# Kernel tuning notes

Hardware: AMD Instinct MI355X
Metric: run time of the kernel (lower is better)

## Reference

```python
import jax, jax.numpy as jnp
import numpy as np

BATCH, N, DIM_IN, DIM_K, DIM_V, NH = 2, 4096, 256, 256, 256, 8

def setup_inputs() -> dict:
    key = jax.random.key(0)
    k1, k2, k3, k4 = jax.random.split(key, 4)
    s = 1.0 / np.sqrt(DIM_IN)
    return {
        "x": jax.random.normal(k1, (BATCH, N, DIM_IN), dtype=jnp.float32),
        "Wq": jax.random.normal(k2, (DIM_IN, DIM_K), dtype=jnp.float32) * s,
        "Wk": jax.random.normal(k3, (DIM_IN, DIM_K), dtype=jnp.float32) * s,
        "Wv": jax.random.normal(k4, (DIM_IN, DIM_V), dtype=jnp.float32) * s,
    }

def reference(x, Wq, Wk, Wv):
    b, n, _ = x.shape
    nh = NH
    dk = DIM_K // nh
    dv = DIM_V // nh
    # project and split heads: [b, nh, n, dk]
    q = jnp.einsum('bni,ik->bnk', x, Wq).reshape(b, n, nh, dk).transpose(0, 2, 1, 3)
    k = jnp.einsum('bni,ik->bnk', x, Wk).reshape(b, n, nh, dk).transpose(0, 2, 1, 3)
    v = jnp.einsum('bni,iv->bnv', x, Wv).reshape(b, n, nh, dv).transpose(0, 2, 1, 3)
    scale = 1.0 / np.sqrt(dk)
    dist = jnp.einsum('bhqd,bhkd->bhqk', q, k) * scale  # [b, nh, n, n]
    dist = jax.nn.softmax(dist, axis=-1)
    # dropout is identity in eval mode
    att = jnp.einsum('bhqk,bhkv->bhqv', dist, v)  # [b, nh, n, dv]
    return att.transpose(0, 2, 1, 3).reshape(b, n, DIM_V)
```

## Files before the change

kernel.cpp:

```cpp
#include <hip/hip_runtime.h>
#include <math.h>

#define BATCH 2
#define SEQ   4096
#define DIN   256
#define NH    8
#define DH    32
#define BH    (BATCH*NH)
#define NSPLIT 4
#define KRANGE (SEQ/NSPLIT)
#define TILES  (KRANGE/64)

typedef short bf16x8 __attribute__((ext_vector_type(8)));
typedef float f32x4  __attribute__((ext_vector_type(4)));

#if defined(__has_builtin)
#if __has_builtin(__builtin_amdgcn_exp2f)
#define EXP2(x) __builtin_amdgcn_exp2f(x)
#else
#define EXP2_ASM 1
#endif
#else
#define EXP2_ASM 1
#endif
#ifdef EXP2_ASM
__device__ __forceinline__ float exp2_raw(float x) {
    float r;
    asm("v_exp_f32 %0, %1\n\ts_nop 1" : "=v"(r) : "v"(x));
    return r;
}
#define EXP2(x) exp2_raw(x)
#endif

#define SC2 0.25508218f

__device__ __forceinline__ unsigned short f2bf(float f) {
    unsigned int u = __builtin_bit_cast(unsigned int, f);
    u += 0x7fffu + ((u >> 16) & 1u);
    return (unsigned short)(u >> 16);
}

__device__ __forceinline__ unsigned int pack_bf2(float f0, float f1) {
    unsigned int u0 = __builtin_bit_cast(unsigned int, f0) + 0x8000u;
    unsigned int u1 = __builtin_bit_cast(unsigned int, f1) + 0x8000u;
    return __builtin_amdgcn_perm(u1, u0, 0x07060302u);
}

__device__ __forceinline__ unsigned int pack_bf2_t(float f0, float f1) {
    return __builtin_amdgcn_perm(__builtin_bit_cast(unsigned int, f1),
                                 __builtin_bit_cast(unsigned int, f0),
                                 0x07060302u);
}

#if defined(__has_builtin)
#if __has_builtin(__builtin_amdgcn_global_load_lds)
#define HAS_ASYNC_LDS 1
#endif
#endif

__device__ __forceinline__ void stage16(const unsigned short* g,
                                        unsigned short* lds_base, int lane) {
#ifdef HAS_ASYNC_LDS
    __builtin_amdgcn_global_load_lds(
        (const __attribute__((address_space(1))) unsigned int*)g,
        (__attribute__((address_space(3))) unsigned int*)lds_base, 16, 0, 0);
#else
    *(bf16x8*)(lds_base + (size_t)lane * 8) = *(const bf16x8*)g;
#endif
}

__global__ __launch_bounds__(256) void prep_kernel(
    const float* __restrict__ x,
    const float* __restrict__ Wq, const float* __restrict__ Wk, const float* __restrict__ Wv,
    unsigned short* __restrict__ xb, unsigned short* __restrict__ Wt)
{
    const int t = threadIdx.x;
    if (blockIdx.x < 2048) {
        int i4 = blockIdx.x * 256 + t;
        float4 v = ((const float4*)x)[i4];
        ushort4 o;
        o.x = f2bf(v.x); o.y = f2bf(v.y); o.z = f2bf(v.z); o.w = f2bf(v.w);
        ((ushort4*)xb)[i4] = o;
    } else {
        __shared__ float ws[64][65];
        int id   = blockIdx.x - 2048;
        int wsel = id >> 4;
        int tile = id & 15;
        int tr = (tile >> 2) * 64;
        int tc = (tile & 3) * 64;
        const float* __restrict__ W = (wsel == 0) ? Wq : (wsel == 1) ? Wk : Wv;
        #pragma unroll
        for (int i = 0; i < 16; i++) {
            int row = i * 4 + (t >> 6), col = t & 63;
            ws[row][col] = W[(size_t)(tr + row) * DIN + tc + col];
        }
        __syncthreads();
        unsigned short* dst = Wt + (size_t)wsel * DIN * DIN;
        #pragma unroll
        for (int i = 0; i < 16; i++) {
            int orow = i * 4 + (t >> 6), ocol = t & 63;
            dst[(size_t)(tc + orow) * DIN + tr + ocol] = f2bf(ws[ocol][orow]);
        }
    }
}

__global__ __launch_bounds__(256) void proj_kernel(
    const unsigned short* __restrict__ xb, const unsigned short* __restrict__ Wt,
    unsigned short* __restrict__ qh, unsigned short* __restrict__ kh,
    unsigned short* __restrict__ vt)
{
    __shared__ __align__(16) unsigned short abuf[8][4][64][8];
    __shared__ __align__(16) unsigned short bbuf[8][4][64][8];

    const int wsel = blockIdx.y;
    const int w    = threadIdx.x >> 6;
    const int lane = threadIdx.x & 63;
    const int quad = lane >> 4;
    const int l16  = lane & 15;

    const int sl   = lane ^ (lane >> 3);
    const int sl16 = sl >> 2, squad = sl & 3;
    const int s_ = (l16 << 2) | quad;
    const int jj = (s_ & 56) | ((s_ ^ (s_ >> 3)) & 7);

    int arow0, brow0;
    const unsigned short *Abase, *Bbase;
    if (wsel < 2) {
        int tt = blockIdx.x >> 7, nt = blockIdx.x & 127;
        arow0 = tt * 64; brow0 = nt * 64;
        Abase = Wt + (size_t)wsel * DIN * DIN + (size_t)arow0 * DIN;
        Bbase = xb + (size_t)brow0 * DIN;
    } else {
        int nt = blockIdx.x >> 2, tt = blockIdx.x & 3;
        arow0 = nt * 64; brow0 = tt * 64;
        Abase = xb + (size_t)arow0 * DIN;
        Bbase = Wt + (size_t)2 * DIN * DIN + (size_t)brow0 * DIN;
    }

    #pragma unroll
    for (int i = 0; i < 16; i++) {
        int id  = w * 16 + i;
        int isB = id >> 5, kb = (id >> 2) & 7, rt = id & 3;
        const unsigned short* src = (isB ? Bbase : Abase)
                                  + (size_t)(rt * 16 + sl16) * DIN + kb * 32 + squad * 8;
        unsigned short* dst = isB ? &bbuf[kb][rt][0][0] : &abuf[kb][rt][0][0];
        stage16(src, dst, lane);
    }
    __syncthreads();

    f32x4 acc[4];
    #pragma unroll
    for (int c = 0; c < 4; c++) acc[c] = (f32x4){0.f, 0.f, 0.f, 0.f};

    #pragma unroll
    for (int kb = 0; kb < 8; kb++) {
        bf16x8 af = *(const bf16x8*)&abuf[kb][w][jj][0];
        #pragma unroll
        for (int c = 0; c < 4; c++) {
            bf16x8 bfr = *(const bf16x8*)&bbuf[kb][c][jj][0];
            acc[c] = __builtin_amdgcn_mfma_f32_16x16x32_bf16(af, bfr, acc[c], 0, 0, 0);
        }
    }

    if (wsel < 2) {
        const float scl = (wsel == 0) ? SC2 : 1.0f;
        unsigned short* __restrict__ dst0 = (wsel == 0) ? qh : kh;
        const int t0 = arow0 + w * 16;
        const int h = t0 >> 5, d0 = (t0 & 31) + quad * 4;
        #pragma unroll
        for (int c = 0; c < 4; c++) {
            int n = brow0 + c * 16 + l16;
            int b = n >> 12, n12 = n & 4095;
            unsigned int u01 = pack_bf2(acc[c][0] * scl, acc[c][1] * scl);
            unsigned int u23 = pack_bf2(acc[c][2] * scl, acc[c][3] * scl);
            *(uint2*)&dst0[((size_t)(b * NH + h) * SEQ + n12) * DH + d0] = make_uint2(u01, u23);
        }
    } else {
        const int n0w = arow0 + w * 16;
        const int b = n0w >> 12, nbase = (n0w & 4095) + quad * 4;
        #pragma unroll
        for (int c = 0; c < 4; c++) {
            int t = brow0 + c * 16;
            int h = t >> 5, d = (t & 31) + l16;
            unsigned int u01 = pack_bf2(acc[c][0], acc[c][1]);
            unsigned int u23 = pack_bf2(acc[c][2], acc[c][3]);
            *(uint2*)&vt[((size_t)(b * NH + h) * DH + d) * SEQ + nbase] = make_uint2(u01, u23);
        }
    }
}

__global__ __launch_bounds__(256, 4) void attn_kernel(
    const unsigned short* __restrict__ qh,
    const unsigned short* __restrict__ kh,
    const unsigned short* __restrict__ vt,
    unsigned short* __restrict__ po, float* __restrict__ pl)
{
    __shared__ __align__(16) unsigned short pbuf[4][16][64];
    __shared__ __align__(16) unsigned short kbuf[2][4][64][8];
    __shared__ __align__(16) unsigned short vbuf[2][4][64][8];

    const int tid  = threadIdx.x;
    const int wave = tid >> 6;
    const int lane = tid & 63;
    const int quad = lane >> 4;
    const int l16  = lane & 15;
    const int sw   = l16 & 7;

    const int bh = blockIdx.x & 15;
    const int qb = (blockIdx.x >> 4) & 31;
    const int ks = blockIdx.x >> 9;
    const int q0 = qb * 128 + wave * 32;
    const int kbase = ks * KRANGE;

    const unsigned short* __restrict__ Qp = qh + (size_t)bh * SEQ * DH;
    const unsigned short* __restrict__ Kp = kh + (size_t)bh * SEQ * DH;
    const unsigned short* __restrict__ Vp = vt + (size_t)bh * DH * SEQ;

    const int sl    = lane ^ (lane >> 3);
    const int sl16  = sl >> 2, squad = sl & 3;
    const unsigned short* ksrc = Kp + (size_t)(kbase + wave * 16 + sl16) * DH + squad * 8;
    const int vdh = wave >> 1, vkh = wave & 1;
    const unsigned short* vsrc = Vp + (size_t)(vdh * 16 + sl16) * SEQ + kbase + vkh * 32 + squad * 8;

    const int s_ = (l16 << 2) | quad;
    const int jj = (s_ & 56) | ((s_ ^ (s_ >> 3)) & 7);

    bf16x8 qf[2];
    qf[0] = *(const bf16x8*)(Qp + (size_t)(q0 +      l16) * DH + quad * 8);
    qf[1] = *(const bf16x8*)(Qp + (size_t)(q0 + 16 + l16) * DH + quad * 8);

    const bf16x8 ones = {0x3F80, 0x3F80, 0x3F80, 0x3F80, 0x3F80, 0x3F80, 0x3F80, 0x3F80};

    f32x4 o[2][2];
    f32x4 lones[2];
    #pragma unroll
    for (int i = 0; i < 2; i++) {
        o[i][0] = (f32x4){0.f, 0.f, 0.f, 0.f};
        o[i][1] = (f32x4){0.f, 0.f, 0.f, 0.f};
        lones[i] = (f32x4){0.f, 0.f, 0.f, 0.f};
    }
    const f32x4 z = {0.f, 0.f, 0.f, 0.f};

    stage16(ksrc, &kbuf[0][wave][0][0], lane);
    stage16(vsrc, &vbuf[0][wave][0][0], lane);
    ksrc += 64 * DH;
    vsrc += 64;

    for (int t = 0; t < TILES; t++) {
        const int buf = t & 1;

        __syncthreads();

        if (t + 1 < TILES) {
            stage16(ksrc, &kbuf[buf ^ 1][wave][0][0], lane);
            stage16(vsrc, &vbuf[buf ^ 1][wave][0][0], lane);
            ksrc += 64 * DH;
            vsrc += 64;
        }

        bf16x8 kf[4], vf[4];
        #pragma unroll
        for (int c = 0; c < 4; c++) kf[c] = *(const bf16x8*)&kbuf[buf][c][jj][0];
        #pragma unroll
        for (int f = 0; f < 4; f++) vf[f] = *(const bf16x8*)&vbuf[buf][f][jj][0];

        #pragma unroll
        for (int qt = 0; qt < 2; qt++) {
            #pragma unroll
            for (int c = 0; c < 4; c++) {
                f32x4 s = __builtin_amdgcn_mfma_f32_16x16x32_bf16(kf[c], qf[qt], z, 0, 0, 0);
                float e0 = EXP2(s[0]);
                float e1 = EXP2(s[1]);
                float e2 = EXP2(s[2]);
                float e3 = EXP2(s[3]);
                int chs = ((c * 2 + (quad >> 1)) ^ sw) * 8 + (quad & 1) * 4;
                *(uint2*)&pbuf[wave][l16][chs] =
                    make_uint2(pack_bf2_t(e0, e1), pack_bf2_t(e2, e3));
            }
            bf16x8 pf0 = *(const bf16x8*)&pbuf[wave][l16][((0 + quad) ^ sw) * 8];
            bf16x8 pf1 = *(const bf16x8*)&pbuf[wave][l16][((4 + quad) ^ sw) * 8];
            o[qt][0] = __builtin_amdgcn_mfma_f32_16x16x32_bf16(pf0, vf[0], o[qt][0], 0, 0, 0);
            o[qt][0] = __builtin_amdgcn_mfma_f32_16x16x32_bf16(pf1, vf[1], o[qt][0], 0, 0, 0);
            o[qt][1] = __builtin_amdgcn_mfma_f32_16x16x32_bf16(pf0, vf[2], o[qt][1], 0, 0, 0);
            o[qt][1] = __builtin_amdgcn_mfma_f32_16x16x32_bf16(pf1, vf[3], o[qt][1], 0, 0, 0);
            lones[qt] = __builtin_amdgcn_mfma_f32_16x16x32_bf16(pf0, ones, lones[qt], 0, 0, 0);
            lones[qt] = __builtin_amdgcn_mfma_f32_16x16x32_bf16(pf1, ones, lones[qt], 0, 0, 0);
        }
    }

    const size_t obase = (size_t)(ks * BH + bh) * SEQ;
    #pragma unroll
    for (int qt = 0; qt < 2; qt++) {
        if (l16 == 0) {
            #pragma unroll
            for (int r = 0; r < 4; r++)
                pl[obase + q0 + qt * 16 + quad * 4 + r] = lones[qt][r];
        }
        #pragma unroll
        for (int r = 0; r < 4; r++) {
            int n = q0 + qt * 16 + quad * 4 + r;
            unsigned short* dst = po + (obase + n) * DH;
            dst[l16]      = f2bf(o[qt][0][r]);
            dst[16 + l16] = f2bf(o[qt][1][r]);
        }
    }
}

__global__ __launch_bounds__(256) void merge_kernel(
    const unsigned short* __restrict__ po, const float* __restrict__ pl,
    float* __restrict__ out)
{
    int t    = blockIdx.x * 256 + threadIdx.x;
    int d8   = t & 7;
    int pair = t >> 3;
    int bh   = pair >> 12;
    int n    = pair & 4095;
    float s0 = 0.f, s1 = 0.f, s2 = 0.f, s3 = 0.f, ls = 0.f;
    #pragma unroll
    for (int sp = 0; sp < NSPLIT; sp++) {
        size_t base = (size_t)(sp * BH + bh) * SEQ + n;
        uint2 v = ((const uint2*)(po + base * DH))[d8];
        s0 += __builtin_bit_cast(float, v.x << 16);
        s1 += __builtin_bit_cast(float, v.x & 0xFFFF0000u);
        s2 += __builtin_bit_cast(float, v.y << 16);
        s3 += __builtin_bit_cast(float, v.y & 0xFFFF0000u);
        ls += pl[base];
    }
    float inv = 1.f / ls;
    int b = bh >> 3, h = bh & 7;
    float4 o = {s0 * inv, s1 * inv, s2 * inv, s3 * inv};
    ((float4*)(out + ((size_t)b * SEQ + n) * (NH * DH) + h * DH))[d8] = o;
}

extern "C" void kernel_launch(void* const* d_in, const int* in_sizes, int n_in,
                              void* d_out, int out_size, void* d_ws, size_t ws_size,
                              hipStream_t stream)
{
    const float* x  = (const float*)d_in[0];
    const float* Wq = (const float*)d_in[1];
    const float* Wk = (const float*)d_in[2];
    const float* Wv = (const float*)d_in[3];
    float* out = (float*)d_out;

    unsigned short* qh = (unsigned short*)d_ws;
    unsigned short* kh = qh + (size_t)BH * SEQ * DH;
    unsigned short* vt = kh + (size_t)BH * SEQ * DH;
    unsigned short* xb = vt + (size_t)BH * SEQ * DH;
    unsigned short* Wt = xb + (size_t)BATCH * SEQ * DIN;
    unsigned short* po = Wt + 3 * DIN * DIN;
    float* pl = (float*)(po + (size_t)NSPLIT * BH * SEQ * DH);

    prep_kernel<<<dim3(2096), 256, 0, stream>>>(x, Wq, Wk, Wv, xb, Wt);
    proj_kernel<<<dim3(512, 3), 256, 0, stream>>>(xb, Wt, qh, kh, vt);
    attn_kernel<<<dim3(BH * (SEQ / 128) * NSPLIT), 256, 0, stream>>>(qh, kh, vt, po, pl);
    merge_kernel<<<dim3(2048), 256, 0, stream>>>(po, pl, out);
}
```

Measured before the change: 137.6 us.

## Fuse x bf16 conversion into projection, halve key splits, double-buffer P tile

Removes the separate x-to-bf16 pass from the prep kernel. The projection kernel now loads fp32 x directly, converts it in registers and writes the bf16 result to LDS. This saves a full write and re-read of a bf16 copy of x, but loses the async global-to-LDS path for the x operand. The key-range split drops from 4 to 2, which halves the attention grid and the partial outputs the merge kernel must read, at the cost of fewer concurrent blocks and longer per-block loops. The P staging buffer in LDS gets a separate slot per query tile, so the two qt iterations no longer reuse the same storage.

Measured after the change: 137.7 us. No clear change (+0.1%).

```diff
diff --git a/kernel.cpp b/kernel.cpp
--- a/kernel.cpp
+++ b/kernel.cpp
@@ -7,7 +7,7 @@
 #define NH    8
 #define DH    32
 #define BH    (BATCH*NH)
-#define NSPLIT 4
+#define NSPLIT 2
 #define KRANGE (SEQ/NSPLIT)
 #define TILES  (KRANGE/64)
 
@@ -70,42 +70,33 @@
 }
 
 __global__ __launch_bounds__(256) void prep_kernel(
-    const float* __restrict__ x,
     const float* __restrict__ Wq, const float* __restrict__ Wk, const float* __restrict__ Wv,
-    unsigned short* __restrict__ xb, unsigned short* __restrict__ Wt)
-{
+    unsigned short* __restrict__ Wt)
+{
+    __shared__ float ws[64][65];
     const int t = threadIdx.x;
-    if (blockIdx.x < 2048) {
-        int i4 = blockIdx.x * 256 + t;
-        float4 v = ((const float4*)x)[i4];
-        ushort4 o;
-        o.x = f2bf(v.x); o.y = f2bf(v.y); o.z = f2bf(v.z); o.w = f2bf(v.w);
-        ((ushort4*)xb)[i4] = o;
-    } else {
-        __shared__ float ws[64][65];
-        int id   = blockIdx.x - 2048;
-        int wsel = id >> 4;
-        int tile = id & 15;
-        int tr = (tile >> 2) * 64;
-        int tc = (tile & 3) * 64;
-        const float* __restrict__ W = (wsel == 0) ? Wq : (wsel == 1) ? Wk : Wv;
-        #pragma unroll
-        for (int i = 0; i < 16; i++) {
-            int row = i * 4 + (t >> 6), col = t & 63;
-            ws[row][col] = W[(size_t)(tr + row) * DIN + tc + col];
-        }
-        __syncthreads();
-        unsigned short* dst = Wt + (size_t)wsel * DIN * DIN;
-        #pragma unroll
-        for (int i = 0; i < 16; i++) {
-            int orow = i * 4 + (t >> 6), ocol = t & 63;
-            dst[(size_t)(tc + orow) * DIN + tr + ocol] = f2bf(ws[ocol][orow]);
-        }
+    int id   = blockIdx.x;
+    int wsel = id >> 4;
+    int tile = id & 15;
+    int tr = (tile >> 2) * 64;
+    int tc = (tile & 3) * 64;
+    const float* __restrict__ W = (wsel == 0) ? Wq : (wsel == 1) ? Wk : Wv;
+    #pragma unroll
+    for (int i = 0; i < 16; i++) {
+        int row = i * 4 + (t >> 6), col = t & 63;
+        ws[row][col] = W[(size_t)(tr + row) * DIN + tc + col];
+    }
+    __syncthreads();
+    unsigned short* dst = Wt + (size_t)wsel * DIN * DIN;
+    #pragma unroll
+    for (int i = 0; i < 16; i++) {
+        int orow = i * 4 + (t >> 6), ocol = t & 63;
+        dst[(size_t)(tc + orow) * DIN + tr + ocol] = f2bf(ws[ocol][orow]);
     }
 }
 
 __global__ __launch_bounds__(256) void proj_kernel(
-    const unsigned short* __restrict__ xb, const unsigned short* __restrict__ Wt,
+    const float* __restrict__ x, const unsigned short* __restrict__ Wt,
     unsigned short* __restrict__ qh, unsigned short* __restrict__ kh,
     unsigned short* __restrict__ vt)
 {
@@ -124,27 +115,41 @@
     const int jj = (s_ & 56) | ((s_ ^ (s_ >> 3)) & 7);
 
     int arow0, brow0;
-    const unsigned short *Abase, *Bbase;
+    const unsigned short* Wbase;
+    const float* Xbase;
+    unsigned short (*wdst)[4][64][8];
+    unsigned short (*xdst)[4][64][8];
     if (wsel < 2) {
         int tt = blockIdx.x >> 7, nt = blockIdx.x & 127;
         arow0 = tt * 64; brow0 = nt * 64;
-        Abase = Wt + (size_t)wsel * DIN * DIN + (size_t)arow0 * DIN;
-        Bbase = xb + (size_t)brow0 * DIN;
+        Wbase = Wt + (size_t)wsel * DIN * DIN + (size_t)arow0 * DIN;
+        Xbase = x + (size_t)brow0 * DIN;
+        wdst = abuf; xdst = bbuf;
     } else {
         int nt = blockIdx.x >> 2, tt = blockIdx.x & 3;
         arow0 = nt * 64; brow0 = tt * 64;
-        Abase = xb + (size_t)arow0 * DIN;
-        Bbase = Wt + (size_t)2 * DIN * DIN + (size_t)brow0 * DIN;
-    }
-
-    #pragma unroll
-    for (int i = 0; i < 16; i++) {
-        int id  = w * 16 + i;
-        int isB = id >> 5, kb = (id >> 2) & 7, rt = id & 3;
-        const unsigned short* src = (isB ? Bbase : Abase)
-                                  + (size_t)(rt * 16 + sl16) * DIN + kb * 32 + squad * 8;
-        unsigned short* dst = isB ? &bbuf[kb][rt][0][0] : &abuf[kb][rt][0][0];
-        stage16(src, dst, lane);
+        Xbase = x + (size_t)arow0 * DIN;
+        Wbase = Wt + (size_t)2 * DIN * DIN + (size_t)brow0 * DIN;
+        wdst = bbuf; xdst = abuf;
+    }
+
+    #pragma unroll
+    for (int i = 0; i < 8; i++) {
+        int id = w * 8 + i;
+        int kb = id >> 2, rt = id & 3;
+        stage16(Wbase + (size_t)(rt * 16 + sl16) * DIN + kb * 32 + squad * 8,
+                &wdst[kb][rt][0][0], lane);
+    }
+    #pragma unroll
+    for (int i = 0; i < 8; i++) {
+        int id = w * 8 + i;
+        int kb = id >> 2, rt = id & 3;
+        const float4* src = (const float4*)(Xbase + (size_t)(rt * 16 + sl16) * DIN
+                                            + kb * 32 + squad * 8);
+        float4 a = src[0], b = src[1];
+        uint4 p = { pack_bf2(a.x, a.y), pack_bf2(a.z, a.w),
+                    pack_bf2(b.x, b.y), pack_bf2(b.z, b.w) };
+        *(uint4*)(&xdst[kb][rt][0][0] + (size_t)lane * 8) = p;
     }
     __syncthreads();
 
@@ -195,7 +200,7 @@
     const unsigned short* __restrict__ vt,
     unsigned short* __restrict__ po, float* __restrict__ pl)
 {
-    __shared__ __align__(16) unsigned short pbuf[4][16][64];
+    __shared__ __align__(16) unsigned short pbuf[4][2][16][64];
     __shared__ __align__(16) unsigned short kbuf[2][4][64][8];
     __shared__ __align__(16) unsigned short vbuf[2][4][64][8];
 
@@ -274,11 +279,11 @@
                 float e2 = EXP2(s[2]);
                 float e3 = EXP2(s[3]);
                 int chs = ((c * 2 + (quad >> 1)) ^ sw) * 8 + (quad & 1) * 4;
-                *(uint2*)&pbuf[wave][l16][chs] =
+                *(uint2*)&pbuf[wave][qt][l16][chs] =
                     make_uint2(pack_bf2_t(e0, e1), pack_bf2_t(e2, e3));
             }
-            bf16x8 pf0 = *(const bf16x8*)&pbuf[wave][l16][((0 + quad) ^ sw) * 8];
-            bf16x8 pf1 = *(const bf16x8*)&pbuf[wave][l16][((4 + quad) ^ sw) * 8];
+            bf16x8 pf0 = *(const bf16x8*)&pbuf[wave][qt][l16][((0 + quad) ^ sw) * 8];
+            bf16x8 pf1 = *(const bf16x8*)&pbuf[wave][qt][l16][((4 + quad) ^ sw) * 8];
             o[qt][0] = __builtin_amdgcn_mfma_f32_16x16x32_bf16(pf0, vf[0], o[qt][0], 0, 0, 0);
             o[qt][0] = __builtin_amdgcn_mfma_f32_16x16x32_bf16(pf1, vf[1], o[qt][0], 0, 0, 0);
             o[qt][1] = __builtin_amdgcn_mfma_f32_16x16x32_bf16(pf0, vf[2], o[qt][1], 0, 0, 0);
@@ -345,13 +350,12 @@
     unsigned short* qh = (unsigned short*)d_ws;
     unsigned short* kh = qh + (size_t)BH * SEQ * DH;
     unsigned short* vt = kh + (size_t)BH * SEQ * DH;
-    unsigned short* xb = vt + (size_t)BH * SEQ * DH;
-    unsigned short* Wt = xb + (size_t)BATCH * SEQ * DIN;
+    unsigned short* Wt = vt + (size_t)BH * SEQ * DH;
     unsigned short* po = Wt + 3 * DIN * DIN;
     float* pl = (float*)(po + (size_t)NSPLIT * BH * SEQ * DH);
 
-    prep_kernel<<<dim3(2096), 256, 0, stream>>>(x, Wq, Wk, Wv, xb, Wt);
-    proj_kernel<<<dim3(512, 3), 256, 0, stream>>>(xb, Wt, qh, kh, vt);
+    prep_kernel<<<dim3(48), 256, 0, stream>>>(Wq, Wk, Wv, Wt);
+    proj_kernel<<<dim3(512, 3), 256, 0, stream>>>(x, Wt, qh, kh, vt);
     attn_kernel<<<dim3(BH * (SEQ / 128) * NSPLIT), 256, 0, stream>>>(qh, kh, vt, po, pl);
     merge_kernel<<<dim3(2048), 256, 0, stream>>>(po, pl, out);
 }
```
